# Optimization experiments

Hardware: AMD Instinct MI355X
Metric: run time of the kernel (lower is better)

## Reference

```python
import jax, jax.numpy as jnp
import numpy as np

N = 80000
E = 1280000
EPS = 1e-5

def _lrelu(x):
    return jax.nn.leaky_relu(x, 0.01)

def _bn(h):
    # training-mode BatchNorm1d with batch size 1: stats over the node dim; affine is identity at init
    return (h - h.mean(0)) / jnp.sqrt(h.var(0) + EPS)

def _ln(h, g, b):
    m = h.mean(-1, keepdims=True)
    v = h.var(-1, keepdims=True)
    return (h - m) / jnp.sqrt(v + EPS) * g + b

def _gcn(h, w, b, src, dst, n):
    # PyG GCNConv: add self loops, symmetric deg^-1/2 normalization, aggregate at target
    hw = h @ w.T
    loop = jnp.arange(n, dtype=src.dtype)
    s = jnp.concatenate([src, loop])
    d = jnp.concatenate([dst, loop])
    deg = jax.ops.segment_sum(jnp.ones(d.shape, hw.dtype), d, num_segments=n)
    dinv = jnp.where(deg > 0, 1.0 / jnp.sqrt(deg), 0.0)
    msg = hw[s] * (dinv[s] * dinv[d])[:, None]  # [E+N, C]
    return jax.ops.segment_sum(msg, d, num_segments=n) + b

def _tnet(x, c1w, c1b, c2w, c2b, c3w, c3b, f1w, f1b, f2w, f2b, f3w, f3b):
    h = jax.nn.relu(x @ c1w.T + c1b)          # [N,64]  (source skips bn1)
    h = jax.nn.relu(_bn(h @ c2w.T + c2b))     # [N,128]
    h = jax.nn.relu(_bn(h @ c3w.T + c3b))     # [N,1024]
    g = h.max(0)                              # global max pool -> [1024]
    g = jax.nn.relu(g @ f1w.T + f1b)
    g = jax.nn.relu(g @ f2w.T + f2b)
    iden = jnp.array([1.0, 0.0, 0.0, 0.0, 1.0, 0.0, 0.0, 0.0, 1.0], x.dtype)
    g = g @ f3w.T + f3b + iden
    return g.reshape(3, 3)

def _forward(edge_index, x, tnet_c1_w, tnet_c1_b, tnet_c2_w, tnet_c2_b, tnet_c3_w, tnet_c3_b, tnet_fc1_w, tnet_fc1_b, tnet_fc2_w, tnet_fc2_b, tnet_fc3_w, tnet_fc3_b, conv1_w, conv1_b, g1_li_w, g1_li_b, g1_gcn_w, g1_gcn_b, g1_ln_g, g1_ln_b, conv2_w, conv2_b, g2_li_w, g2_li_b, g2_gcn_w, g2_gcn_b, g2_ln_g, g2_ln_b, conv3_w, conv3_b, out_w, out_b):
    src, dst = edge_index[0], edge_index[1]
    n = x.shape[0]
    T = _tnet(x, tnet_c1_w, tnet_c1_b, tnet_c2_w, tnet_c2_b, tnet_c3_w, tnet_c3_b, tnet_fc1_w, tnet_fc1_b, tnet_fc2_w, tnet_fc2_b, tnet_fc3_w, tnet_fc3_b)
    h0 = x @ T                                  # [N,3] spatial transform
    xg = _lrelu(h0 @ conv1_w.T + conv1_b)       # [N,64] (conv1d k=1 == per-node linear)
    # Gcn_Attention 1
    nf = _lrelu(xg @ g1_li_w.T + g1_li_b)
    nf2 = _lrelu(_gcn(nf, g1_gcn_w, g1_gcn_b, src, dst, n))
    h = _ln(jnp.concatenate([nf, nf2], 1), g1_ln_g, g1_ln_b)   # [N,128]
    h = _lrelu(h @ conv2_w.T + conv2_b)
    # Gcn_Attention 2
    nf = _lrelu(h @ g2_li_w.T + g2_li_b)
    nf2 = _lrelu(_gcn(nf, g2_gcn_w, g2_gcn_b, src, dst, n))
    h = _ln(jnp.concatenate([nf, nf2], 1), g2_ln_g, g2_ln_b)   # [N,256]
    h = jnp.concatenate([h, xg], 1)                            # [N,320]
    h = _lrelu(h @ conv3_w.T + conv3_b)                        # [N,256]
    pooled = h.mean(0)                                         # global mean pool (single graph)
    feat = jnp.concatenate([jnp.broadcast_to(pooled, (n, pooled.shape[0])), xg], 1)  # [N,320]
    return feat @ out_w.T + out_b                              # [N,4]

def setup_inputs():
    ki = iter(jax.random.split(jax.random.key(0), 32))
    def W(shape):
        return jax.random.normal(next(ki), shape, jnp.float32) * (1.0 / float(np.sqrt(shape[-1])))
    z = lambda n: jnp.zeros((n,), jnp.float32)
    o = lambda n: jnp.ones((n,), jnp.float32)
    inp = {}
    inp['x'] = jax.random.normal(next(ki), (N, 3), jnp.float32)
    inp['edge_index'] = jax.random.randint(next(ki), (2, E), 0, N, dtype=jnp.int32)
    inp['tnet_c1_w'] = W((64, 3)); inp['tnet_c1_b'] = z(64)
    inp['tnet_c2_w'] = W((128, 64)); inp['tnet_c2_b'] = z(128)
    inp['tnet_c3_w'] = W((1024, 128)); inp['tnet_c3_b'] = z(1024)
    inp['tnet_fc1_w'] = W((512, 1024)); inp['tnet_fc1_b'] = z(512)
    inp['tnet_fc2_w'] = W((256, 512)); inp['tnet_fc2_b'] = z(256)
    inp['tnet_fc3_w'] = W((9, 256)); inp['tnet_fc3_b'] = z(9)
    inp['conv1_w'] = W((64, 3)); inp['conv1_b'] = z(64)
    inp['g1_li_w'] = W((64, 64)); inp['g1_li_b'] = z(64)
    inp['g1_gcn_w'] = W((64, 64)); inp['g1_gcn_b'] = z(64)
    inp['g1_ln_g'] = o(128); inp['g1_ln_b'] = z(128)
    inp['conv2_w'] = W((128, 128)); inp['conv2_b'] = z(128)
    inp['g2_li_w'] = W((128, 128)); inp['g2_li_b'] = z(128)
    inp['g2_gcn_w'] = W((128, 128)); inp['g2_gcn_b'] = z(128)
    inp['g2_ln_g'] = o(256); inp['g2_ln_b'] = z(256)
    inp['conv3_w'] = W((256, 320)); inp['conv3_b'] = z(256)
    inp['out_w'] = W((4, 320)); inp['out_b'] = z(4)
    return inp

def reference(x, edge_index, tnet_c1_w, tnet_c1_b, tnet_c2_w, tnet_c2_b, tnet_c3_w, tnet_c3_b, tnet_fc1_w, tnet_fc1_b, tnet_fc2_w, tnet_fc2_b, tnet_fc3_w, tnet_fc3_b, conv1_w, conv1_b, g1_li_w, g1_li_b, g1_gcn_w, g1_gcn_b, g1_ln_g, g1_ln_b, conv2_w, conv2_b, g2_li_w, g2_li_b, g2_gcn_w, g2_gcn_b, g2_ln_g, g2_ln_b, conv3_w, conv3_b, out_w, out_b):
    return _forward(edge_index, x, tnet_c1_w, tnet_c1_b, tnet_c2_w, tnet_c2_b, tnet_c3_w, tnet_c3_b, tnet_fc1_w, tnet_fc1_b, tnet_fc2_w, tnet_fc2_b, tnet_fc3_w, tnet_fc3_b, conv1_w, conv1_b, g1_li_w, g1_li_b, g1_gcn_w, g1_gcn_b, g1_ln_g, g1_ln_b, conv2_w, conv2_b, g2_li_w, g2_li_b, g2_gcn_w, g2_gcn_b, g2_ln_g, g2_ln_b, conv3_w, conv3_b, out_w, out_b)
```

## Files before the change

### kernel.cpp

```cpp
#include <hip/hip_runtime.h>
#include <cstddef>

#define EPSV 1e-5f

typedef __attribute__((ext_vector_type(8))) short frag8;
typedef __attribute__((ext_vector_type(4))) float f32x4;

__device__ __forceinline__ float lrelu01(float v) { return v > 0.f ? v : 0.01f * v; }
__device__ __forceinline__ void atomAddF(float* p, float v) { unsafeAtomicAdd(p, v); }
__device__ __forceinline__ unsigned fkey(float f) {
    unsigned u = __float_as_uint(f);
    return (u & 0x80000000u) ? ~u : (u | 0x80000000u);
}
__device__ __forceinline__ unsigned short f2b(float f) {
    unsigned u = __float_as_uint(f);
    unsigned r = u + 0x7fffu + ((u >> 16) & 1u);
    return (unsigned short)(r >> 16);
}
__device__ __forceinline__ float b2f(unsigned short h) {
    return __uint_as_float(((unsigned)h) << 16);
}
__device__ __forceinline__ float blo(unsigned u) { return __uint_as_float(u << 16); }
__device__ __forceinline__ float bhi(unsigned u) { return __uint_as_float(u & 0xffff0000u); }

static inline unsigned cdivu(unsigned a, unsigned b) { return (a + b - 1) / b; }


__global__ void k_degrank(const int* __restrict__ dst, int* __restrict__ deg,
                          int* __restrict__ rank, int E) {
    int e = blockIdx.x * 256 + threadIdx.x;
    if (e < E) rank[e] = atomicAdd(&deg[dst[e]], 1);
}

__global__ void k_scan_local(const int* __restrict__ deg, int* __restrict__ startv,
                             int* __restrict__ bsum, float* __restrict__ dinv, int n) {
    __shared__ int t0[256];
    int tid = threadIdx.x;
    int i = blockIdx.x * 256 + tid;
    int v = (i < n) ? deg[i] : 0;
    if (i < n) dinv[i] = rsqrtf((float)(v + 1));
    t0[tid] = v;
    __syncthreads();
    for (int o = 1; o < 256; o <<= 1) {
        int add = (tid >= o) ? t0[tid - o] : 0;
        __syncthreads();
        t0[tid] += add;
        __syncthreads();
    }
    if (i < n) startv[i] = t0[tid] - v;
    if (tid == 255) bsum[blockIdx.x] = t0[255];
}

__global__ void k_scan_bsum(int* __restrict__ bsum, int nb) {
    __shared__ int t0[512];
    int tid = threadIdx.x;
    int v = (tid < nb) ? bsum[tid] : 0;
    t0[tid] = v;
    __syncthreads();
    for (int o = 1; o < 512; o <<= 1) {
        int add = (tid >= o) ? t0[tid - o] : 0;
        __syncthreads();
        t0[tid] += add;
        __syncthreads();
    }
    if (tid < nb) bsum[tid] = t0[tid] - v;
}

__global__ void k_scan_add(int* __restrict__ startv, const int* __restrict__ bsum, int n) {
    int i = blockIdx.x * 256 + threadIdx.x;
    if (i < n) startv[i] += bsum[blockIdx.x];
}

__global__ void k_fill(const int* __restrict__ src, const int* __restrict__ dst,
                       const int* __restrict__ rank, const int* __restrict__ startv,
                       int* __restrict__ csr, int E) {
    int e = blockIdx.x * 256 + threadIdx.x;
    if (e < E) csr[startv[dst[e]] + rank[e]] = src[e];
}

template <int CH>
__launch_bounds__(256)
__global__ void k_gln(const int* __restrict__ startv, const int* __restrict__ degv,
                      const int* __restrict__ csr, const unsigned short* __restrict__ q,
                      const unsigned short* __restrict__ nf, const float* __restrict__ dinv,
                      const float* __restrict__ gcn_b, const float* __restrict__ lng,
                      const float* __restrict__ lnb, unsigned short* __restrict__ outp,
                      int ldo, int n) {
    const int wv = threadIdx.x >> 6, lane = threadIdx.x & 63;
    const int g = lane >> 4, p = lane & 15;
    int node = blockIdx.x * 4 + wv;
    if (node >= n) return;
    constexpr int CPL = CH / 16;
    constexpr int DPL = CPL / 2;

    float acc[CPL];
#pragma unroll
    for (int k = 0; k < CPL; ++k) acc[k] = 0.f;

    {
        unsigned su[DPL];
        const unsigned short* qrow = q + (size_t)node * CH + p * CPL;
        if (DPL == 4) *(uint4*)su = *(const uint4*)qrow;
        else          *(uint2*)su = *(const uint2*)qrow;
        if (g == 0) {
#pragma unroll
            for (int d = 0; d < DPL; ++d) { acc[2 * d] += blo(su[d]); acc[2 * d + 1] += bhi(su[d]); }
        }
    }

    int s0 = startv[node], cnt = degv[node];
    int sidx[4];
#pragma unroll
    for (int t = 0; t < 4; ++t) { int j = t * 4 + g; sidx[t] = (j < cnt) ? csr[s0 + j] : 0; }
    for (int j0 = 0; j0 < cnt; j0 += 16) {
        unsigned buf[4][DPL];
#pragma unroll
        for (int t = 0; t < 4; ++t) {
            const unsigned short* src = q + (size_t)sidx[t] * CH + p * CPL;
            if (DPL == 4) *(uint4*)buf[t] = *(const uint4*)src;
            else          *(uint2*)buf[t] = *(const uint2*)src;
        }
        int nsidx[4];
#pragma unroll
        for (int t = 0; t < 4; ++t) {
            int j = j0 + 16 + t * 4 + g;
            nsidx[t] = (j < cnt) ? csr[s0 + j] : 0;
        }
#pragma unroll
        for (int t = 0; t < 4; ++t) {
            if (j0 + t * 4 + g < cnt) {
#pragma unroll
                for (int d = 0; d < DPL; ++d) {
                    acc[2 * d] += blo(buf[t][d]);
                    acc[2 * d + 1] += bhi(buf[t][d]);
                }
            }
        }
#pragma unroll
        for (int t = 0; t < 4; ++t) sidx[t] = nsidx[t];
    }

#pragma unroll
    for (int k = 0; k < CPL; ++k) {
        acc[k] += __shfl_xor(acc[k], 16);
        acc[k] += __shfl_xor(acc[k], 32);
    }

    float di = dinv[node];
    float nv[CPL], bv[CPL];
    {
        unsigned su[DPL];
        const unsigned short* nrow = nf + (size_t)node * CH + p * CPL;
        if (DPL == 4) *(uint4*)su = *(const uint4*)nrow;
        else          *(uint2*)su = *(const uint2*)nrow;
#pragma unroll
        for (int d = 0; d < DPL; ++d) { nv[2 * d] = blo(su[d]); nv[2 * d + 1] = bhi(su[d]); }
    }
    const float* gb = gcn_b + p * CPL;
#pragma unroll
    for (int k = 0; k < CPL; ++k) bv[k] = lrelu01(di * acc[k] + gb[k]);

    float s = 0.f, ss = 0.f;
#pragma unroll
    for (int k = 0; k < CPL; ++k) { s += nv[k] + bv[k]; ss += nv[k] * nv[k] + bv[k] * bv[k]; }
#pragma unroll
    for (int off = 32; off > 0; off >>= 1) { s += __shfl_xor(s, off); ss += __shfl_xor(ss, off); }
    const float inv = 1.f / (float)(8 * CH);
    float mu = s * inv;
    float var = ss * inv - mu * mu;
    float rsg = rsqrtf(var + EPSV);

    unsigned short* orow = outp + (size_t)node * ldo;
    if (g == 0) {
        unsigned short tmp[CPL];
        const float* lg = lng + p * CPL; const float* lb = lnb + p * CPL;
#pragma unroll
        for (int k = 0; k < CPL; ++k) tmp[k] = f2b((nv[k] - mu) * rsg * lg[k] + lb[k]);
        if (DPL == 4) *(uint4*)(orow + p * CPL) = *(uint4*)tmp;
        else          *(uint2*)(orow + p * CPL) = *(uint2*)tmp;
    } else if (g == 1) {
        unsigned short tmp[CPL];
        const float* lg = lng + CH + p * CPL; const float* lb = lnb + CH + p * CPL;
#pragma unroll
        for (int k = 0; k < CPL; ++k) tmp[k] = f2b((bv[k] - mu) * rsg * lg[k] + lb[k]);
        if (DPL == 4) *(uint4*)(orow + CH + p * CPL) = *(uint4*)tmp;
        else          *(uint2*)(orow + CH + p * CPL) = *(uint2*)tmp;
    }
}


__global__ void k_wconv(const float* __restrict__ s0, const float* __restrict__ s1,
                        const float* __restrict__ s2, const float* __restrict__ s3,
                        const float* __restrict__ s4, const float* __restrict__ s5,
                        const float* __restrict__ s6, const float* __restrict__ s7,
                        unsigned short* __restrict__ dst) {
    int t = blockIdx.x * 256 + threadIdx.x;
    if (t >= 278528) return;
    const float* srcs[8] = {s0, s1, s2, s3, s4, s5, s6, s7};
    const int off[9] = {0, 8192, 139264, 143360, 147456, 163840, 180224, 196608, 278528};
    int seg = 0;
    while (t >= off[seg + 1]) ++seg;
    dst[t] = f2b(srcs[seg][t - off[seg]]);
}

__global__ void k_h1(const float* __restrict__ x, const float* __restrict__ w,
                     const float* __restrict__ b, unsigned short* __restrict__ h1, int n) {
    int node = blockIdx.x * 256 + threadIdx.x;
    if (node >= n) return;
    float x0 = x[node * 3], x1 = x[node * 3 + 1], x2 = x[node * 3 + 2];
    unsigned short* o = h1 + (size_t)node * 64;
#pragma unroll
    for (int cp = 0; cp < 8; ++cp) {
        unsigned short tmp[8];
#pragma unroll
        for (int t = 0; t < 8; ++t) {
            int c = cp * 8 + t;
            float v = x0 * w[c * 3] + x1 * w[c * 3 + 1] + x2 * w[c * 3 + 2] + b[c];
            tmp[t] = f2b(fmaxf(v, 0.f));
        }
        *(float4*)(o + cp * 8) = *(float4*)tmp;
    }
}

__global__ void k_prebn(const float* __restrict__ z, const float* __restrict__ sum2,
                        const float* __restrict__ ss2, unsigned short* __restrict__ a3,
                        int total, float invn) {
    int t = (blockIdx.x * 256 + threadIdx.x) * 4;
    if (t >= total) return;
    int c = t & 127;
    float4 v = *(const float4*)(z + t);
    float vv[4] = {v.x, v.y, v.z, v.w};
    unsigned short o[4];
#pragma unroll
    for (int i = 0; i < 4; ++i) {
        float m = sum2[c + i] * invn;
        float var = ss2[c + i] * invn - m * m;
        o[i] = f2b(fmaxf((vv[i] - m) * rsqrtf(var + EPSV), 0.f));
    }
    *(ushort4*)(a3 + t) = *(ushort4*)o;
}

__launch_bounds__(256)
__global__ void k_fc1(const float* __restrict__ sum3, const float* __restrict__ ss3,
                      const unsigned* __restrict__ maxk,
                      const float* __restrict__ f1w, const float* __restrict__ f1b,
                      float* __restrict__ a1, float invn) {
    __shared__ float g[1024];
    int tid = threadIdx.x;
    for (int c = tid; c < 1024; c += 256) {
        float m = sum3[c] * invn;
        float var = ss3[c] * invn - m * m;
        unsigned k = maxk[c];
        unsigned u = (k & 0x80000000u) ? (k & 0x7FFFFFFFu) : ~k;
        g[c] = fmaxf((__uint_as_float(u) - m) * rsqrtf(var + EPSV), 0.f);
    }
    __syncthreads();
    int row = blockIdx.x * 64 + (tid >> 2);
    int part = tid & 3;
    const float* w = f1w + (size_t)row * 1024 + part * 256;
    const float* gg = g + part * 256;
    float s = 0.f;
    for (int k = 0; k < 256; ++k) s = fmaf(w[k], gg[k], s);
    s += __shfl_xor(s, 1); s += __shfl_xor(s, 2);
    if (part == 0) a1[row] = fmaxf(s + f1b[row], 0.f);
}

__launch_bounds__(256)
__global__ void k_fc23(const float* __restrict__ a1, const float* __restrict__ f2w,
                       const float* __restrict__ f2b, const float* __restrict__ f3w,
                       const float* __restrict__ f3b, float* __restrict__ T9) {
    __shared__ float a2[256];
    int tid = threadIdx.x;
    {
        const float* w = f2w + (size_t)tid * 512;
        float s = f2b[tid];
        for (int k = 0; k < 512; ++k) s = fmaf(w[k], a1[k], s);
        a2[tid] = fmaxf(s, 0.f);
    }
    __syncthreads();
    if (tid < 9) {
        const float* w = f3w + (size_t)tid * 256;
        float s = f3b[tid];
        for (int k = 0; k < 256; ++k) s = fmaf(w[k], a2[k], s);
        if (tid == 0 || tid == 4 || tid == 8) s += 1.f;
        T9[tid] = s;
    }
}

__global__ void k_xg(const float* __restrict__ x, const float* __restrict__ T9,
                     const float* __restrict__ w, const float* __restrict__ b,
                     unsigned short* __restrict__ xg, int n) {
    int node = blockIdx.x * 256 + threadIdx.x;
    if (node >= n) return;
    float x0 = x[node * 3], x1 = x[node * 3 + 1], x2 = x[node * 3 + 2];
    float h0 = x0 * T9[0] + x1 * T9[3] + x2 * T9[6];
    float h1 = x0 * T9[1] + x1 * T9[4] + x2 * T9[7];
    float h2 = x0 * T9[2] + x1 * T9[5] + x2 * T9[8];
    unsigned short* o = xg + (size_t)node * 320;
#pragma unroll
    for (int cp = 0; cp < 8; ++cp) {
        unsigned short tmp[8];
#pragma unroll
        for (int t = 0; t < 8; ++t) {
            int c = cp * 8 + t;
            float v = h0 * w[c * 3] + h1 * w[c * 3 + 1] + h2 * w[c * 3 + 2] + b[c];
            tmp[t] = f2b(lrelu01(v));
        }
        *(float4*)(o + cp * 8) = *(float4*)tmp;
    }
}

__global__ void k_const4(const float* __restrict__ pooled, const float* __restrict__ ow,
                         const float* __restrict__ ob, float* __restrict__ c4, float invn) {
    int j = threadIdx.x >> 6, lane = threadIdx.x & 63;
    float s = 0.f;
    for (int c = lane; c < 256; c += 64) s += pooled[c] * invn * ow[j * 320 + c];
#pragma unroll
    for (int off = 32; off > 0; off >>= 1) s += __shfl_down(s, off);
    if (lane == 0) c4[j] = s + ob[j];
}

__global__ void k_out(const unsigned short* __restrict__ hcat, const float* __restrict__ ow,
                      const float* __restrict__ c4, float* __restrict__ out, int n) {
    int node = blockIdx.x * 256 + threadIdx.x;
    if (node >= n) return;
    const unsigned short* xgp = hcat + (size_t)node * 320 + 256;
    float s0 = c4[0], s1 = c4[1], s2 = c4[2], s3 = c4[3];
#pragma unroll
    for (int cp = 0; cp < 8; ++cp) {
        float4 raw = *(const float4*)(xgp + cp * 8);
        unsigned short tmp[8];
        *(float4*)tmp = raw;
#pragma unroll
        for (int t = 0; t < 8; ++t) {
            int k = 256 + cp * 8 + t;
            float f = b2f(tmp[t]);
            s0 = fmaf(f, ow[k], s0);
            s1 = fmaf(f, ow[320 + k], s1);
            s2 = fmaf(f, ow[640 + k], s2);
            s3 = fmaf(f, ow[960 + k], s3);
        }
    }
    *(float4*)(out + (size_t)node * 4) = make_float4(s0, s1, s2, s3);
}

enum { MF_BIAS = 1, MF_LRELU = 2, MF_DINV = 4, MF_STOREF = 8, MF_STOREB = 16,
       MF_STATS = 32, MF_COLSUM = 64 };

template <int BN, int MODE>
__launch_bounds__(256)
__global__ void k_mgemm(const unsigned short* __restrict__ A, int lda, int K,
                        const unsigned short* __restrict__ W,
                        const float* __restrict__ bias,
                        float* __restrict__ OutF, unsigned short* __restrict__ OutB, int ldo,
                        const float* __restrict__ dinv,
                        float* __restrict__ sum_o, float* __restrict__ ss_o,
                        unsigned* __restrict__ maxk_o) {
    constexpr int BM = 128;
    constexpr int LDT = 40;
    __shared__ unsigned short As[BM * LDT];
    __shared__ unsigned short Ws[BN * LDT];
    __shared__ float redS[2 * 128];
    __shared__ unsigned redM[128];

    const int tid = threadIdx.x;
    const int wid = tid >> 6, lane = tid & 63;
    const int quad = lane >> 4, lrow = lane & 15;
    const int bn0 = blockIdx.x * BM;
    const int bc0 = blockIdx.y * BN;

    constexpr int NI = (BN == 128) ? 4 : 2;
    constexpr int NJ = 4;
    const int wm = (BN == 128) ? (wid & 1) * 64 : wid * 32;
    const int wn = (BN == 128) ? (wid >> 1) * 64 : 0;

    if (MODE & (MF_STATS | MF_COLSUM)) {
        for (int c = tid; c < BN; c += 256) {
            redS[c] = 0.f; redS[128 + c] = 0.f; redM[c] = 0u;
        }
    }

    f32x4 acc[NI][NJ] = {};

    for (int k0 = 0; k0 < K; k0 += 32) {
#pragma unroll
        for (int h = 0; h < 2; ++h) {
            int ch = tid + h * 256;
            int row = ch >> 2, cp = ch & 3;
            const unsigned short* src = A + (size_t)(bn0 + row) * lda + k0 + cp * 8;
            *(float4*)&As[row * LDT + cp * 8] = *(const float4*)src;
        }
#pragma unroll
        for (int h = 0; h < BN / 64; ++h) {
            int ch = tid + h * 256;
            int row = ch >> 2, cp = ch & 3;
            const unsigned short* src = W + (size_t)(bc0 + row) * K + k0 + cp * 8;
            *(float4*)&Ws[row * LDT + cp * 8] = *(const float4*)src;
        }
        __syncthreads();
        frag8 af[NI], bf[NJ];
#pragma unroll
        for (int i = 0; i < NI; ++i)
            af[i] = *(const frag8*)&As[(wm + i * 16 + lrow) * LDT + quad * 8];
#pragma unroll
        for (int j = 0; j < NJ; ++j)
            bf[j] = *(const frag8*)&Ws[(wn + j * 16 + lrow) * LDT + quad * 8];
#pragma unroll
        for (int i = 0; i < NI; ++i)
#pragma unroll
            for (int j = 0; j < NJ; ++j)
                acc[i][j] = __builtin_amdgcn_mfma_f32_16x16x32_bf16(af[i], bf[j], acc[i][j], 0, 0, 0);
        __syncthreads();
    }

#pragma unroll
    for (int j = 0; j < NJ; ++j) {
        const int col = bc0 + wn + j * 16 + lrow;
        float bv = (MODE & MF_BIAS) ? bias[col] : 0.f;
        float s = 0.f, q = 0.f, m = -3.4e38f;
#pragma unroll
        for (int i = 0; i < NI; ++i) {
            const int rowb = bn0 + wm + i * 16 + quad * 4;
#pragma unroll
            for (int r = 0; r < 4; ++r) {
                float t = acc[i][j][r] + bv;
                if (MODE & MF_LRELU) t = lrelu01(t);
                if (MODE & MF_DINV) t *= dinv[rowb + r];
                if (MODE & MF_STOREF) OutF[(size_t)(rowb + r) * ldo + col] = t;
                if (MODE & MF_STOREB) OutB[(size_t)(rowb + r) * ldo + col] = f2b(t);
                s += t; q += t * t; m = fmaxf(m, t);
            }
        }
        if (MODE & (MF_STATS | MF_COLSUM)) {
            s += __shfl_xor(s, 16); s += __shfl_xor(s, 32);
            if (MODE & MF_STATS) {
                q += __shfl_xor(q, 16); q += __shfl_xor(q, 32);
                m = fmaxf(m, __shfl_xor(m, 16)); m = fmaxf(m, __shfl_xor(m, 32));
            }
            if (quad == 0) {
                int lc = wn + j * 16 + lrow;
                atomicAdd(&redS[lc], s);
                if (MODE & MF_STATS) {
                    atomicAdd(&redS[128 + lc], q);
                    atomicMax(&redM[lc], fkey(m));
                }
            }
        }
    }
    if (MODE & (MF_STATS | MF_COLSUM)) {
        __syncthreads();
        for (int c = tid; c < BN; c += 256) {
            atomAddF(&sum_o[bc0 + c], redS[c]);
            if (MODE & MF_STATS) {
                atomAddF(&ss_o[bc0 + c], redS[128 + c]);
                atomicMax(&maxk_o[bc0 + c], redM[c]);
            }
        }
    }
}

template <int BN>
__launch_bounds__(256)
__global__ void k_ligc(const unsigned short* __restrict__ A, int lda, int K,
                       const unsigned short* __restrict__ Wli, const float* __restrict__ bli,
                       const unsigned short* __restrict__ Wgc, const float* __restrict__ dinv,
                       unsigned short* __restrict__ NF, int ldnf,
                       unsigned short* __restrict__ Q, int ldq) {
    constexpr int BM = 128;
    constexpr int LDT = 40;
    constexpr int LDT2 = BN + 8;
    __shared__ unsigned short SA[BM * LDT2];
    __shared__ unsigned short Ws[BN * LDT];

    const int tid = threadIdx.x;
    const int wid = tid >> 6, lane = tid & 63;
    const int quad = lane >> 4, lrow = lane & 15;
    const int bn0 = blockIdx.x * BM;
    constexpr int NI = (BN == 128) ? 4 : 2;
    constexpr int NJ = 4;
    const int wm = (BN == 128) ? (wid & 1) * 64 : wid * 32;
    const int wn = (BN == 128) ? (wid >> 1) * 64 : 0;

    {
        f32x4 acc[NI][NJ] = {};
        for (int k0 = 0; k0 < K; k0 += 32) {
#pragma unroll
            for (int h = 0; h < 2; ++h) {
                int ch = tid + h * 256;
                int row = ch >> 2, cp = ch & 3;
                *(float4*)&SA[row * LDT + cp * 8] =
                    *(const float4*)(A + (size_t)(bn0 + row) * lda + k0 + cp * 8);
            }
#pragma unroll
            for (int h = 0; h < BN / 64; ++h) {
                int ch = tid + h * 256;
                int row = ch >> 2, cp = ch & 3;
                *(float4*)&Ws[row * LDT + cp * 8] =
                    *(const float4*)(Wli + (size_t)row * K + k0 + cp * 8);
            }
            __syncthreads();
            frag8 af[NI], bf[NJ];
#pragma unroll
            for (int i = 0; i < NI; ++i)
                af[i] = *(const frag8*)&SA[(wm + i * 16 + lrow) * LDT + quad * 8];
#pragma unroll
            for (int j = 0; j < NJ; ++j)
                bf[j] = *(const frag8*)&Ws[(wn + j * 16 + lrow) * LDT + quad * 8];
#pragma unroll
            for (int i = 0; i < NI; ++i)
#pragma unroll
                for (int j = 0; j < NJ; ++j)
                    acc[i][j] = __builtin_amdgcn_mfma_f32_16x16x32_bf16(af[i], bf[j], acc[i][j], 0, 0, 0);
            __syncthreads();
        }
#pragma unroll
        for (int j = 0; j < NJ; ++j) {
            const int col = wn + j * 16 + lrow;
            float bv = bli[col];
#pragma unroll
            for (int i = 0; i < NI; ++i) {
                const int rowl = wm + i * 16 + quad * 4;
#pragma unroll
                for (int r = 0; r < 4; ++r) {
                    unsigned short h = f2b(lrelu01(acc[i][j][r] + bv));
                    NF[(size_t)(bn0 + rowl + r) * ldnf + col] = h;
                    SA[(rowl + r) * LDT2 + col] = h;
                }
            }
        }
        __syncthreads();
    }
    {
        f32x4 acc[NI][NJ] = {};
        for (int k0 = 0; k0 < BN; k0 += 32) {
#pragma unroll
            for (int h = 0; h < BN / 64; ++h) {
                int ch = tid + h * 256;
                int row = ch >> 2, cp = ch & 3;
                *(float4*)&Ws[row * LDT + cp * 8] =
                    *(const float4*)(Wgc + (size_t)row * BN + k0 + cp * 8);
            }
            __syncthreads();
            frag8 af[NI], bf[NJ];
#pragma unroll
            for (int i = 0; i < NI; ++i)
                af[i] = *(const frag8*)&SA[(wm + i * 16 + lrow) * LDT2 + k0 + quad * 8];
#pragma unroll
            for (int j = 0; j < NJ; ++j)
                bf[j] = *(const frag8*)&Ws[(wn + j * 16 + lrow) * LDT + quad * 8];
#pragma unroll
            for (int i = 0; i < NI; ++i)
#pragma unroll
                for (int j = 0; j < NJ; ++j)
                    acc[i][j] = __builtin_amdgcn_mfma_f32_16x16x32_bf16(af[i], bf[j], acc[i][j], 0, 0, 0);
            __syncthreads();
        }
#pragma unroll
        for (int j = 0; j < NJ; ++j) {
            const int col = wn + j * 16 + lrow;
#pragma unroll
            for (int i = 0; i < NI; ++i) {
                const int rowb = bn0 + wm + i * 16 + quad * 4;
#pragma unroll
                for (int r = 0; r < 4; ++r) {
                    float t = acc[i][j][r] * dinv[rowb + r];
                    Q[(size_t)(rowb + r) * ldq + col] = f2b(t);
                }
            }
        }
    }
}

__launch_bounds__(256)
__global__ void k_z3(const unsigned short* __restrict__ A,
                     const unsigned short* __restrict__ W,
                     const float* __restrict__ bias,
                     float* __restrict__ sum_o, float* __restrict__ ss_o,
                     unsigned* __restrict__ maxk_o, int ntiles) {
    __shared__ unsigned short As[128 * 128];
    __shared__ unsigned short Ws[128 * 128];
    const int tid = threadIdx.x;
    const int wid = tid >> 6, lane = tid & 63;
    const int quad = lane >> 4, lrow = lane & 15;

    int bid = blockIdx.x;
    int w = (bid & 7) * ntiles + (bid >> 3);
    const int bn0 = (w >> 3) * 128;
    const int bc0 = (w & 7) * 128;

#pragma unroll
    for (int h = 0; h < 8; ++h) {
        int flat = h * 256 + tid;
        int l = flat & 63, kc = (flat >> 6) & 3, r16 = flat >> 8;
        int row = r16 * 16 + (l & 15), k0 = kc * 32 + (l >> 4) * 8;
        *(float4*)&As[flat * 8] = *(const float4*)(A + (size_t)(bn0 + row) * 128 + k0);
        *(float4*)&Ws[flat * 8] = *(const float4*)(W + (size_t)(bc0 + row) * 128 + k0);
    }
    __syncthreads();

    const int ar = (wid & 1) * 4;
    const int wc = (wid >> 1) * 4;
    f32x4 acc[4][4] = {};
#pragma unroll
    for (int kc = 0; kc < 4; ++kc) {
        frag8 af[4], bf[4];
#pragma unroll
        for (int i = 0; i < 4; ++i)
            af[i] = *(const frag8*)&As[(((ar + i) * 4 + kc) * 64 + lane) * 8];
#pragma unroll
        for (int j = 0; j < 4; ++j)
            bf[j] = *(const frag8*)&Ws[(((wc + j) * 4 + kc) * 64 + lane) * 8];
#pragma unroll
        for (int i = 0; i < 4; ++i)
#pragma unroll
            for (int j = 0; j < 4; ++j)
                acc[i][j] = __builtin_amdgcn_mfma_f32_16x16x32_bf16(af[i], bf[j], acc[i][j], 0, 0, 0);
    }

#pragma unroll
    for (int j = 0; j < 4; ++j) {
        int c = bc0 + (wc + j) * 16 + lrow;
        float bv = bias[c];
        float s = 0.f, q = 0.f, m = -3.4e38f;
#pragma unroll
        for (int i = 0; i < 4; ++i)
#pragma unroll
            for (int r = 0; r < 4; ++r) {
                float t = acc[i][j][r] + bv;
                s += t; q += t * t; m = fmaxf(m, t);
            }
        s += __shfl_xor(s, 16); s += __shfl_xor(s, 32);
        q += __shfl_xor(q, 16); q += __shfl_xor(q, 32);
        m = fmaxf(m, __shfl_xor(m, 16)); m = fmaxf(m, __shfl_xor(m, 32));
        if (quad == 0) {
            atomAddF(&sum_o[c], s);
            atomAddF(&ss_o[c], q);
            atomicMax(&maxk_o[c], fkey(m));
        }
    }
}


extern "C" void kernel_launch(void* const* d_in, const int* in_sizes, int n_in,
                              void* d_out, int out_size, void* d_ws, size_t ws_size,
                              hipStream_t stream) {
    const float* x   = (const float*)d_in[0];
    const int*   ei  = (const int*)d_in[1];
    const float* c1w = (const float*)d_in[2];  const float* c1b = (const float*)d_in[3];
    const float* c2w = (const float*)d_in[4];  const float* c2b = (const float*)d_in[5];
    const float* c3w = (const float*)d_in[6];  const float* c3b = (const float*)d_in[7];
    const float* f1w = (const float*)d_in[8];  const float* f1b = (const float*)d_in[9];
    const float* f2w = (const float*)d_in[10]; const float* f2b = (const float*)d_in[11];
    const float* f3w = (const float*)d_in[12]; const float* f3b = (const float*)d_in[13];
    const float* cv1w = (const float*)d_in[14]; const float* cv1b = (const float*)d_in[15];
    const float* li1w = (const float*)d_in[16]; const float* li1b = (const float*)d_in[17];
    const float* gc1w = (const float*)d_in[18]; const float* gc1b = (const float*)d_in[19];
    const float* ln1g = (const float*)d_in[20]; const float* ln1b = (const float*)d_in[21];
    const float* cv2w = (const float*)d_in[22]; const float* cv2b = (const float*)d_in[23];
    const float* li2w = (const float*)d_in[24]; const float* li2b = (const float*)d_in[25];
    const float* gc2w = (const float*)d_in[26]; const float* gc2b = (const float*)d_in[27];
    const float* ln2g = (const float*)d_in[28]; const float* ln2b = (const float*)d_in[29];
    const float* cv3w = (const float*)d_in[30]; const float* cv3b = (const float*)d_in[31];
    const float* ow  = (const float*)d_in[32]; const float* ob  = (const float*)d_in[33];
    float* out = (float*)d_out;

    const int N = in_sizes[0] / 3;
    const int E = in_sizes[1] / 2;
    const int* srcI = ei;
    const int* dstI = ei + E;

    char* base = (char*)d_ws;
    size_t off = 0;
    auto take = [&](size_t bytes) -> char* {
        char* p = base + off;
        off = (off + bytes + 255) & ~(size_t)255;
        return p;
    };
    int*   deg    = (int*)  take((size_t)N * 4);
    float* dinv   = (float*)take((size_t)N * 4);
    int*   startv = (int*)  take((size_t)N * 4);
    int*   rank   = (int*)  take((size_t)E * 4);
    int*   csr    = (int*)  take((size_t)E * 4);
    int*   bsum   = (int*)  take(512 * 4);
    float* sm     = (float*)take(8192 * 4);
    unsigned short* WB = (unsigned short*)take(278528 * 2);
    unsigned short* H  = (unsigned short*)take((size_t)N * 320 * 2);
    float* F1 = (float*)take((size_t)N * 128 * 4);
    unsigned short* B1 = (unsigned short*)take((size_t)N * 64 * 2);
    unsigned short* B2 = (unsigned short*)take((size_t)N * 128 * 2);
    unsigned short* B3 = (unsigned short*)take((size_t)N * 128 * 2);

    unsigned short* c2wb  = WB + 0;
    unsigned short* c3wb  = WB + 8192;
    unsigned short* li1wb = WB + 139264;
    unsigned short* gc1wb = WB + 143360;
    unsigned short* cv2wb = WB + 147456;
    unsigned short* li2wb = WB + 163840;
    unsigned short* gc2wb = WB + 180224;
    unsigned short* cv3wb = WB + 196608;

    float* sum2 = sm + 0;    float* ss2 = sm + 128;
    float* sum3 = sm + 256;  float* ss3 = sm + 1280;
    unsigned* maxk = (unsigned*)(sm + 2304);
    float* pooled = sm + 3328;
    unsigned* dmax = (unsigned*)(sm + 3584);
    float* T9  = sm + 3968; float* c4 = sm + 3984;
    float* a1  = sm + 5120;

    const float invn = 1.0f / (float)N;
    const dim3 blk(256);
    const unsigned GX = (unsigned)(N / 128);
    const unsigned NB = cdivu((unsigned)N, 256);

    hipMemsetAsync(deg, 0, (size_t)N * 4, stream);
    hipMemsetAsync(sm, 0, 3712 * 4, stream);

    k_degrank<<<cdivu(E, 256), blk, 0, stream>>>(dstI, deg, rank, E);
    k_scan_local<<<NB, blk, 0, stream>>>(deg, startv, bsum, dinv, N);
    k_scan_bsum<<<1, 512, 0, stream>>>(bsum, (int)NB);
    k_scan_add<<<NB, blk, 0, stream>>>(startv, bsum, N);
    k_fill<<<cdivu(E, 256), blk, 0, stream>>>(srcI, dstI, rank, startv, csr, E);

    k_wconv<<<cdivu(278528, 256), blk, 0, stream>>>(c2w, c3w, li1w, gc1w, cv2w, li2w, gc2w, cv3w, WB);

    k_h1<<<cdivu((unsigned)N, 256), blk, 0, stream>>>(x, c1w, c1b, B1, N);
    k_mgemm<128, (MF_BIAS | MF_STOREF | MF_STATS)><<<dim3(GX, 1), blk, 0, stream>>>(
        B1, 64, 64, c2wb, c2b, F1, nullptr, 128, nullptr, sum2, ss2, dmax);
    k_prebn<<<cdivu((unsigned)N * 128 / 4, 256), blk, 0, stream>>>(F1, sum2, ss2, B2, N * 128, invn);
    k_z3<<<8 * GX, blk, 0, stream>>>(B2, c3wb, c3b, sum3, ss3, maxk, (int)GX);
    k_fc1<<<8, blk, 0, stream>>>(sum3, ss3, maxk, f1w, f1b, a1, invn);
    k_fc23<<<1, blk, 0, stream>>>(a1, f2w, f2b, f3w, f3b, T9);
    k_xg<<<cdivu((unsigned)N, 256), blk, 0, stream>>>(x, T9, cv1w, cv1b, H + 256, N);

    k_ligc<64><<<GX, blk, 0, stream>>>(H + 256, 320, 64, li1wb, li1b, gc1wb, dinv, B1, 64, B2, 64);
    k_gln<64><<<cdivu((unsigned)N, 4), blk, 0, stream>>>(
        startv, deg, csr, B2, B1, dinv, gc1b, ln1g, ln1b, B3, 128, N);
    k_mgemm<128, (MF_BIAS | MF_LRELU | MF_STOREB)><<<dim3(GX, 1), blk, 0, stream>>>(
        B3, 128, 128, cv2wb, cv2b, nullptr, B2, 128, nullptr, nullptr, nullptr, nullptr);

    k_ligc<128><<<GX, blk, 0, stream>>>(B2, 128, 128, li2wb, li2b, gc2wb, dinv, B3, 128, B2, 128);
    k_gln<128><<<cdivu((unsigned)N, 4), blk, 0, stream>>>(
        startv, deg, csr, B2, B3, dinv, gc2b, ln2g, ln2b, H, 320, N);

    k_mgemm<128, (MF_BIAS | MF_LRELU | MF_COLSUM)><<<dim3(GX, 2), blk, 0, stream>>>(
        H, 320, 320, cv3wb, cv3b, nullptr, nullptr, 0, nullptr, pooled, nullptr, nullptr);

    k_const4<<<1, 256, 0, stream>>>(pooled, ow, ob, c4, invn);
    k_out<<<cdivu((unsigned)N, 256), blk, 0, stream>>>(H, ow, c4, out, N);
}
```

Before: 565.7 us.

## Pre-swizzle z3 operands into MFMA fragment order and drop LDS staging

The producer kernels (k_prebn for activations, k_wconv for the conv3 weight) now write their outputs directly in the per-tile MFMA fragment layout. k_z3 then loads fragments straight from global memory instead of copying 128x128 tiles into shared memory and synchronising. This removes the LDS round trip and barrier, and the 64KB of LDS per block, which should allow more blocks per CU. The cost is that each block's fragment loads now go to global memory, relying on the cache for reuse across the 8 column blocks. The activation writes in k_prebn also become scattered.

Measured after the change: 544.2 us. 1.04x faster.

```diff
diff --git a/kernel.cpp b/kernel.cpp
--- a/kernel.cpp
+++ b/kernel.cpp
@@ -200,7 +200,16 @@
     const int off[9] = {0, 8192, 139264, 143360, 147456, 163840, 180224, 196608, 278528};
     int seg = 0;
     while (t >= off[seg + 1]) ++seg;
-    dst[t] = f2b(srcs[seg][t - off[seg]]);
+    unsigned short v = f2b(srcs[seg][t - off[seg]]);
+    if (seg == 1) {
+        int li = t - 8192;
+        int rch = li >> 7, k = li & 127;
+        int cb = rch >> 7, r = rch & 127;
+        int flat = ((r >> 4) * 4 + (k >> 5)) * 64 + ((k >> 3) & 3) * 16 + (r & 15);
+        dst[8192 + cb * 16384 + flat * 8 + (k & 7)] = v;
+    } else {
+        dst[t] = v;
+    }
 }
 
 __global__ void k_h1(const float* __restrict__ x, const float* __restrict__ w,
@@ -223,21 +232,26 @@
 }
 
 __global__ void k_prebn(const float* __restrict__ z, const float* __restrict__ sum2,
-                        const float* __restrict__ ss2, unsigned short* __restrict__ a3,
-                        int total, float invn) {
-    int t = (blockIdx.x * 256 + threadIdx.x) * 4;
-    if (t >= total) return;
-    int c = t & 127;
-    float4 v = *(const float4*)(z + t);
-    float vv[4] = {v.x, v.y, v.z, v.w};
-    unsigned short o[4];
-#pragma unroll
-    for (int i = 0; i < 4; ++i) {
+                        const float* __restrict__ ss2, unsigned short* __restrict__ a3f,
+                        int n16, float invn) {
+    int t = blockIdx.x * 256 + threadIdx.x;
+    if (t >= n16) return;
+    int row = t >> 4, cp = t & 15;
+    int c = cp * 8;
+    const float* src = z + (size_t)row * 128 + c;
+    float4 v0 = *(const float4*)src;
+    float4 v1 = *(const float4*)(src + 4);
+    float vv[8] = {v0.x, v0.y, v0.z, v0.w, v1.x, v1.y, v1.z, v1.w};
+    unsigned short o[8];
+#pragma unroll
+    for (int i = 0; i < 8; ++i) {
         float m = sum2[c + i] * invn;
         float var = ss2[c + i] * invn - m * m;
         o[i] = f2b(fmaxf((vv[i] - m) * rsqrtf(var + EPSV), 0.f));
     }
-    *(ushort4*)(a3 + t) = *(ushort4*)o;
+    int tile = row >> 7, r = row & 127;
+    int flat = ((r >> 4) * 4 + (cp >> 2)) * 64 + (cp & 3) * 16 + (r & 15);
+    *(float4*)(a3f + (size_t)tile * 16384 + flat * 8) = *(float4*)o;
 }
 
 __launch_bounds__(256)
@@ -572,31 +586,21 @@
 }
 
 __launch_bounds__(256)
-__global__ void k_z3(const unsigned short* __restrict__ A,
-                     const unsigned short* __restrict__ W,
+__global__ void k_z3(const unsigned short* __restrict__ AF,
+                     const unsigned short* __restrict__ WF,
                      const float* __restrict__ bias,
                      float* __restrict__ sum_o, float* __restrict__ ss_o,
                      unsigned* __restrict__ maxk_o, int ntiles) {
-    __shared__ unsigned short As[128 * 128];
-    __shared__ unsigned short Ws[128 * 128];
     const int tid = threadIdx.x;
     const int wid = tid >> 6, lane = tid & 63;
     const int quad = lane >> 4, lrow = lane & 15;
 
     int bid = blockIdx.x;
     int w = (bid & 7) * ntiles + (bid >> 3);
-    const int bn0 = (w >> 3) * 128;
-    const int bc0 = (w & 7) * 128;
-
-#pragma unroll
-    for (int h = 0; h < 8; ++h) {
-        int flat = h * 256 + tid;
-        int l = flat & 63, kc = (flat >> 6) & 3, r16 = flat >> 8;
-        int row = r16 * 16 + (l & 15), k0 = kc * 32 + (l >> 4) * 8;
-        *(float4*)&As[flat * 8] = *(const float4*)(A + (size_t)(bn0 + row) * 128 + k0);
-        *(float4*)&Ws[flat * 8] = *(const float4*)(W + (size_t)(bc0 + row) * 128 + k0);
-    }
-    __syncthreads();
+    const int tile = w >> 3;
+    const int cb = w & 7;
+    const unsigned short* At = AF + (size_t)tile * 16384;
+    const unsigned short* Wt = WF + (size_t)cb * 16384;
 
     const int ar = (wid & 1) * 4;
     const int wc = (wid >> 1) * 4;
@@ -606,10 +610,10 @@
         frag8 af[4], bf[4];
 #pragma unroll
         for (int i = 0; i < 4; ++i)
-            af[i] = *(const frag8*)&As[(((ar + i) * 4 + kc) * 64 + lane) * 8];
+            af[i] = *(const frag8*)&At[(((ar + i) * 4 + kc) * 64 + lane) * 8];
 #pragma unroll
         for (int j = 0; j < 4; ++j)
-            bf[j] = *(const frag8*)&Ws[(((wc + j) * 4 + kc) * 64 + lane) * 8];
+            bf[j] = *(const frag8*)&Wt[(((wc + j) * 4 + kc) * 64 + lane) * 8];
 #pragma unroll
         for (int i = 0; i < 4; ++i)
 #pragma unroll
@@ -619,7 +623,7 @@
 
 #pragma unroll
     for (int j = 0; j < 4; ++j) {
-        int c = bc0 + (wc + j) * 16 + lrow;
+        int c = cb * 128 + (wc + j) * 16 + lrow;
         float bv = bias[c];
         float s = 0.f, q = 0.f, m = -3.4e38f;
 #pragma unroll
@@ -691,7 +695,7 @@
     unsigned short* B3 = (unsigned short*)take((size_t)N * 128 * 2);
 
     unsigned short* c2wb  = WB + 0;
-    unsigned short* c3wb  = WB + 8192;
+    unsigned short* c3wf  = WB + 8192;
     unsigned short* li1wb = WB + 139264;
     unsigned short* gc1wb = WB + 143360;
     unsigned short* cv2wb = WB + 147456;
@@ -726,8 +730,8 @@
     k_h1<<<cdivu((unsigned)N, 256), blk, 0, stream>>>(x, c1w, c1b, B1, N);
     k_mgemm<128, (MF_BIAS | MF_STOREF | MF_STATS)><<<dim3(GX, 1), blk, 0, stream>>>(
         B1, 64, 64, c2wb, c2b, F1, nullptr, 128, nullptr, sum2, ss2, dmax);
-    k_prebn<<<cdivu((unsigned)N * 128 / 4, 256), blk, 0, stream>>>(F1, sum2, ss2, B2, N * 128, invn);
-    k_z3<<<8 * GX, blk, 0, stream>>>(B2, c3wb, c3b, sum3, ss3, maxk, (int)GX);
+    k_prebn<<<cdivu((unsigned)N * 16, 256), blk, 0, stream>>>(F1, sum2, ss2, B2, N * 16, invn);
+    k_z3<<<8 * GX, blk, 0, stream>>>(B2, c3wf, c3b, sum3, ss3, maxk, (int)GX);
     k_fc1<<<8, blk, 0, stream>>>(sum3, ss3, maxk, f1w, f1b, a1, invn);
     k_fc23<<<1, blk, 0, stream>>>(a1, f2w, f2b, f3w, f3b, T9);
     k_xg<<<cdivu((unsigned)N, 256), blk, 0, stream>>>(x, T9, cv1w, cv1b, H + 256, N);
```
